# Kernel tuning notes

Measured on AMD Instinct MI355X. Metric: run time of the kernel, lower is better.

## Reference

```python
import jax, jax.numpy as jnp
import numpy as np

N_NODES = 100000
N_EDGES = 1600000
IN_CH = 128
NHIDDEN = 64
OUT_CH = 40
NLAYERS = 4
ALPHA = 0.1


def setup_inputs() -> dict:
    key = jax.random.key(0)
    ks = jax.random.split(key, 7)
    x = jax.random.normal(ks[0], (N_NODES, IN_CH), dtype=jnp.float32)
    edge_index = jax.random.randint(ks[1], (2, N_EDGES), 0, N_NODES, dtype=jnp.int64)
    batch_graph = jnp.zeros((N_NODES,), dtype=jnp.int64)
    fc1_w = jax.random.normal(ks[2], (NHIDDEN, IN_CH), dtype=jnp.float32) * (1.0 / np.sqrt(IN_CH))
    fc1_b = jax.random.normal(ks[3], (NHIDDEN,), dtype=jnp.float32) * 0.01
    conv_w = jax.random.normal(ks[4], (NLAYERS, NHIDDEN, NHIDDEN), dtype=jnp.float32) * (1.0 / np.sqrt(NHIDDEN))
    fc2_w = jax.random.normal(ks[5], (OUT_CH, NHIDDEN), dtype=jnp.float32) * (1.0 / np.sqrt(NHIDDEN))
    fc2_b = jax.random.normal(ks[6], (OUT_CH,), dtype=jnp.float32) * 0.01
    return {"x": x, "edge_index": edge_index, "batch_graph": batch_graph,
            "fc1_w": fc1_w, "fc1_b": fc1_b, "conv_w": conv_w,
            "fc2_w": fc2_w, "fc2_b": fc2_b}


def reference(x, edge_index, batch_graph, fc1_w, fc1_b, conv_w, fc2_w, fc2_b):
    # eval mode: dropout layers are identity
    n = x.shape[0]
    row, col = edge_index[0], edge_index[1]  # source, target

    # gcn_norm with add_self_loops=False: sym deg^-1/2 normalization
    deg = jax.ops.segment_sum(jnp.ones_like(row, dtype=x.dtype), col, num_segments=n)
    dinv = jnp.where(deg > 0, deg ** -0.5, 0.0)
    norm = (dinv[row] * dinv[col])[:, None]  # [E, 1]

    h = jax.nn.relu(x @ fc1_w.T + fc1_b)  # [N, nhidden]
    h0 = h
    nlayers = conv_w.shape[0]
    for i in range(nlayers):
        # GCN2Conv: aggregate, initial-residual mix, weight1 matmul (beta=1)
        agg = jax.ops.segment_sum(h[row] * norm, col, num_segments=n)
        mixed = (1.0 - ALPHA) * agg + ALPHA * h0
        h = jax.nn.relu(mixed @ conv_w[i])
    out = h @ fc2_w.T + fc2_b  # [N, out_channels]
    return out
```

## Files before the change

### kernel.cpp

```cpp
#include <hip/hip_runtime.h>
#include <hip/hip_fp16.h>

#define N_NODES 100000
#define N_EDGES 1600000
#define IN_CH   128
#define NHID    64
#define OUT_CH  40
#define NBLK    391
#define NBUCK   196
#define BCAP    8960


__global__ __launch_bounds__(256) void k_scan1(const int* __restrict__ cnt,
                                               int* __restrict__ rowptr,
                                               int* __restrict__ bsum) {
    __shared__ int s[256];
    int t = threadIdx.x;
    int n = blockIdx.x * 256 + t;
    int v = (n < N_NODES) ? cnt[n] : 0;
    s[t] = v;
    __syncthreads();
    for (int off = 1; off < 256; off <<= 1) {
        int add = (t >= off) ? s[t - off] : 0;
        __syncthreads();
        s[t] += add;
        __syncthreads();
    }
    int incl = s[t];
    if (n < N_NODES) rowptr[n] = incl - v;
    if (t == 255) bsum[blockIdx.x] = incl;
}

__global__ __launch_bounds__(512) void k_scan2(int* __restrict__ bsum) {
    __shared__ int s[512];
    int t = threadIdx.x;
    int v = (t < NBLK) ? bsum[t] : 0;
    s[t] = v;
    __syncthreads();
    for (int off = 1; off < 512; off <<= 1) {
        int add = (t >= off) ? s[t - off] : 0;
        __syncthreads();
        s[t] += add;
        __syncthreads();
    }
    if (t < NBLK) bsum[t] = s[t] - v;
}

__global__ __launch_bounds__(256) void k_scan3(const int* __restrict__ cnt,
                                               const int* __restrict__ bsum,
                                               int* __restrict__ rowptr,
                                               float* __restrict__ dinv) {
    int n = blockIdx.x * 256 + threadIdx.x;
    if (n < N_NODES) {
        int rp = rowptr[n] + bsum[n >> 8];
        rowptr[n] = rp;
        int c = cnt[n];
        dinv[n] = (c > 0) ? rsqrtf((float)c) : 0.0f;
    }
    if (blockIdx.x == 0 && threadIdx.x == 0) rowptr[N_NODES] = N_EDGES;
}


__global__ __launch_bounds__(256) void k_scatA(const int* __restrict__ ei,
                                               int* __restrict__ bucketCnt,
                                               int2* __restrict__ ebufA) {
    __shared__ int hist[NBUCK];
    __shared__ int base[NBUCK];
    int t = threadIdx.x;
    int chunk = blockIdx.x * 4096;
    for (int i = t; i < NBUCK; i += 256) hist[i] = 0;
    __syncthreads();
#pragma unroll 4
    for (int i = 0; i < 16; i++) {
        int e = chunk + i * 256 + t;
        if (e < N_EDGES) atomicAdd(&hist[ei[N_EDGES + e] >> 9], 1);
    }
    __syncthreads();
    for (int b = t; b < NBUCK; b += 256) {
        int h = hist[b];
        base[b] = h ? atomicAdd(&bucketCnt[b], h) : 0;
    }
    __syncthreads();
#pragma unroll 4
    for (int i = 0; i < 16; i++) {
        int e = chunk + i * 256 + t;
        if (e < N_EDGES) {
            int r = ei[e], c = ei[N_EDGES + e];
            int pos = atomicAdd(&base[c >> 9], 1);
            ebufA[(size_t)(c >> 9) * BCAP + pos] = make_int2(r, c);
        }
    }
}


__global__ __launch_bounds__(256) void k_deg(const int2* __restrict__ ebufA,
                                             const int* __restrict__ bucketCnt,
                                             int* __restrict__ cnt) {
    __shared__ int hist[512];
    int b = blockIdx.x;
    int nodeB = b * 512;
    int t = threadIdx.x;
    for (int i = t; i < 512; i += 256) hist[i] = 0;
    __syncthreads();
    int nE = bucketCnt[b];
    const int2* src = ebufA + (size_t)b * BCAP;
    for (int i = t; i < nE; i += 256) atomicAdd(&hist[src[i].y - nodeB], 1);
    __syncthreads();
    for (int i = t; i < 512; i += 256) {
        int node = nodeB + i;
        if (node < N_NODES) cnt[node] = hist[i];
    }
}


__global__ __launch_bounds__(256) void k_scatB(const int2* __restrict__ ebufA,
                                               const int* __restrict__ bucketCnt,
                                               const float* __restrict__ dinv,
                                               const int* __restrict__ rowptr,
                                               int2* __restrict__ e8) {
    __shared__ int lcur[512];
    int b = blockIdx.x;
    int nodeB = b * 512;
    int t = threadIdx.x;
    for (int i = t; i < 512; i += 256) {
        int node = nodeB + i;
        lcur[i] = (node < N_NODES) ? rowptr[node] : 0;
    }
    __syncthreads();
    int nE = bucketCnt[b];
    const int2* src = ebufA + (size_t)b * BCAP;
    for (int i = t; i < nE; i += 256) {
        int2 rc = src[i];
        float w = dinv[rc.x] * dinv[rc.y];
        int pos = atomicAdd(&lcur[rc.y - nodeB], 1);
        e8[pos] = make_int2(rc.x, __float_as_int(w));
    }
}

__device__ __forceinline__ void store_h4(__half* dst, float a, float b, float c, float d) {
    union { uint2 u; __half2 h[2]; } pk;
    pk.h[0] = __floats2half2_rn(a, b);
    pk.h[1] = __floats2half2_rn(c, d);
    *(uint2*)dst = pk.u;
}


__global__ __launch_bounds__(256, 4) void k_fc1(const float* __restrict__ x,
                                                const float* __restrict__ w,
                                                const float* __restrict__ b,
                                                float* __restrict__ h0,
                                                __half* __restrict__ h016) {
    __shared__ float xs[64 * 128];
    int t = threadIdx.x;
    int nodeBase = blockIdx.x * 64;

    {
        int nl = t >> 2, seg = t & 3;
        int n = nodeBase + nl;
        int swz = (nl >> 2) & 7;
        float4* dstrow = (float4*)(xs + nl * 128);
        if (n < N_NODES) {
            const float4* src = (const float4*)(x + (size_t)n * IN_CH + seg * 32);
#pragma unroll
            for (int q = 0; q < 8; q++) dstrow[(seg * 8 + q) ^ swz] = src[q];
        } else {
            float4 z = {0.f, 0.f, 0.f, 0.f};
#pragma unroll
            for (int q = 0; q < 8; q++) dstrow[(seg * 8 + q) ^ swz] = z;
        }
    }
    __syncthreads();

    int tx = t & 15, ty = t >> 4;
    int n0 = tx * 4, o0 = ty * 4;
    int swz = tx & 7;
    const float4* xrow0 = (const float4*)(xs + (n0 + 0) * 128);
    const float4* xrow1 = (const float4*)(xs + (n0 + 1) * 128);
    const float4* xrow2 = (const float4*)(xs + (n0 + 2) * 128);
    const float4* xrow3 = (const float4*)(xs + (n0 + 3) * 128);

    float c[4][4];
#pragma unroll
    for (int i = 0; i < 4; i++)
#pragma unroll
        for (int j = 0; j < 4; j++) c[i][j] = 0.f;

#pragma unroll 4
    for (int k = 0; k < IN_CH; k += 4) {
        int kg = (k >> 2) ^ swz;
        float4 b0 = *(const float4*)&w[(size_t)(o0 + 0) * IN_CH + k];
        float4 b1 = *(const float4*)&w[(size_t)(o0 + 1) * IN_CH + k];
        float4 b2 = *(const float4*)&w[(size_t)(o0 + 2) * IN_CH + k];
        float4 b3 = *(const float4*)&w[(size_t)(o0 + 3) * IN_CH + k];
        float4 a0 = xrow0[kg];
        float4 a1 = xrow1[kg];
        float4 a2 = xrow2[kg];
        float4 a3 = xrow3[kg];
#pragma unroll
        for (int i = 0; i < 4; i++) {
            float4 a = (i == 0) ? a0 : (i == 1) ? a1 : (i == 2) ? a2 : a3;
            c[i][0] = fmaf(a.x, b0.x, fmaf(a.y, b0.y, fmaf(a.z, b0.z, fmaf(a.w, b0.w, c[i][0]))));
            c[i][1] = fmaf(a.x, b1.x, fmaf(a.y, b1.y, fmaf(a.z, b1.z, fmaf(a.w, b1.w, c[i][1]))));
            c[i][2] = fmaf(a.x, b2.x, fmaf(a.y, b2.y, fmaf(a.z, b2.z, fmaf(a.w, b2.w, c[i][2]))));
            c[i][3] = fmaf(a.x, b3.x, fmaf(a.y, b3.y, fmaf(a.z, b3.z, fmaf(a.w, b3.w, c[i][3]))));
        }
    }

    float4 bias = *(const float4*)&b[o0];
#pragma unroll
    for (int i = 0; i < 4; i++) {
        int n = nodeBase + n0 + i;
        if (n < N_NODES) {
            float4 v;
            v.x = fmaxf(c[i][0] + bias.x, 0.f);
            v.y = fmaxf(c[i][1] + bias.y, 0.f);
            v.z = fmaxf(c[i][2] + bias.z, 0.f);
            v.w = fmaxf(c[i][3] + bias.w, 0.f);
            *(float4*)&h0[(size_t)n * NHID + o0] = v;
            store_h4(&h016[(size_t)n * NHID + o0], v.x, v.y, v.z, v.w);
        }
    }
}


__global__ __launch_bounds__(256, 4) void k_conv(const __half* __restrict__ hin,
                                                 const float* __restrict__ h0,
                                                 const int* __restrict__ rowptr,
                                                 const int2* __restrict__ e8,
                                                 const float* __restrict__ W,
                                                 __half* __restrict__ hout) {
    __shared__ float mix[32 * 68];
    int t = threadIdx.x;
    int nodeBase = blockIdx.x * 32;
    int grp = t >> 3;
    int cg = (t & 7) * 8;

    int n = nodeBase + grp;
    int s = rowptr[n], e = rowptr[n + 1];
    int d = e - s;
    int hi = (d > 0) ? (e - 1) : 0;

    float acc[8];
#pragma unroll
    for (int i = 0; i < 8; i++) acc[i] = 0.f;

    int2  pm[4];
    float4 pv[4];
    if (d > 0) {
#pragma unroll
        for (int u = 0; u < 4; u++) pm[u] = e8[min(s + u, hi)];
#pragma unroll
        for (int u = 0; u < 4; u++) pv[u] = *(const float4*)&hin[(size_t)pm[u].x * NHID + cg];
    }

    for (int j = s; j < e; j += 4) {
        int2  cm[4];
        float4 cv[4];
#pragma unroll
        for (int u = 0; u < 4; u++) { cm[u] = pm[u]; cv[u] = pv[u]; }
        int jn = j + 4;
        if (jn < e) {
#pragma unroll
            for (int u = 0; u < 4; u++) pm[u] = e8[min(jn + u, hi)];
#pragma unroll
            for (int u = 0; u < 4; u++) pv[u] = *(const float4*)&hin[(size_t)pm[u].x * NHID + cg];
        }
#pragma unroll
        for (int u = 0; u < 4; u++) {
            float wgt = (j + u < e) ? __int_as_float(cm[u].y) : 0.f;
            const __half2* hp = (const __half2*)&cv[u];
#pragma unroll
            for (int q = 0; q < 4; q++) {
                float2 f = __half22float2(hp[q]);
                acc[q * 2 + 0] = fmaf(wgt, f.x, acc[q * 2 + 0]);
                acc[q * 2 + 1] = fmaf(wgt, f.y, acc[q * 2 + 1]);
            }
        }
    }

    {
        float4 h0a = *(const float4*)&h0[(size_t)n * NHID + cg];
        float4 h0b = *(const float4*)&h0[(size_t)n * NHID + cg + 4];
        float4 m0, m1;
        m0.x = fmaf(0.9f, acc[0], 0.1f * h0a.x);
        m0.y = fmaf(0.9f, acc[1], 0.1f * h0a.y);
        m0.z = fmaf(0.9f, acc[2], 0.1f * h0a.z);
        m0.w = fmaf(0.9f, acc[3], 0.1f * h0a.w);
        m1.x = fmaf(0.9f, acc[4], 0.1f * h0b.x);
        m1.y = fmaf(0.9f, acc[5], 0.1f * h0b.y);
        m1.z = fmaf(0.9f, acc[6], 0.1f * h0b.z);
        m1.w = fmaf(0.9f, acc[7], 0.1f * h0b.w);
        *(float4*)&mix[grp * 68 + cg] = m0;
        *(float4*)&mix[grp * 68 + cg + 4] = m1;
    }
    __syncthreads();

    int tx = t & 15, ty = t >> 4;
    int o0 = tx * 4, r0 = ty * 2;
    float c[2][4];
#pragma unroll
    for (int i = 0; i < 2; i++)
#pragma unroll
        for (int j = 0; j < 4; j++) c[i][j] = 0.f;

#pragma unroll 4
    for (int k = 0; k < NHID; k += 4) {
        float4 b0 = *(const float4*)&W[(k + 0) * NHID + o0];
        float4 b1 = *(const float4*)&W[(k + 1) * NHID + o0];
        float4 b2 = *(const float4*)&W[(k + 2) * NHID + o0];
        float4 b3 = *(const float4*)&W[(k + 3) * NHID + o0];
#pragma unroll
        for (int i = 0; i < 2; i++) {
            float4 a = *(const float4*)&mix[(r0 + i) * 68 + k];
            c[i][0] = fmaf(a.x, b0.x, fmaf(a.y, b1.x, fmaf(a.z, b2.x, fmaf(a.w, b3.x, c[i][0]))));
            c[i][1] = fmaf(a.x, b0.y, fmaf(a.y, b1.y, fmaf(a.z, b2.y, fmaf(a.w, b3.y, c[i][1]))));
            c[i][2] = fmaf(a.x, b0.z, fmaf(a.y, b1.z, fmaf(a.z, b2.z, fmaf(a.w, b3.z, c[i][2]))));
            c[i][3] = fmaf(a.x, b0.w, fmaf(a.y, b1.w, fmaf(a.z, b2.w, fmaf(a.w, b3.w, c[i][3]))));
        }
    }
#pragma unroll
    for (int i = 0; i < 2; i++) {
        int n2 = nodeBase + r0 + i;
        store_h4(&hout[(size_t)n2 * NHID + o0],
                 fmaxf(c[i][0], 0.f), fmaxf(c[i][1], 0.f),
                 fmaxf(c[i][2], 0.f), fmaxf(c[i][3], 0.f));
    }
}


__global__ __launch_bounds__(256) void k_fc2(const __half* __restrict__ h,
                                             const float* __restrict__ w,
                                             const float* __restrict__ b,
                                             float* __restrict__ out) {
    __shared__ float wT[NHID * 44];
    __shared__ float hs[64 * 68];
    int t = threadIdx.x;
    int nodeBase = blockIdx.x * 64;

    for (int id = t; id < NHID * OUT_CH; id += 256) {
        int o = id >> 6, k = id & 63;
        wT[k * 44 + o] = w[id];
    }
    {
        int nl = t >> 2, seg = t & 3;
        int n = nodeBase + nl;
        float* dst = hs + nl * 68 + seg * 16;
        if (n < N_NODES) {
            float4 raw0 = *(const float4*)&h[(size_t)n * NHID + seg * 16];
            float4 raw1 = *(const float4*)&h[(size_t)n * NHID + seg * 16 + 8];
            const __half2* hp0 = (const __half2*)&raw0;
            const __half2* hp1 = (const __half2*)&raw1;
#pragma unroll
            for (int q = 0; q < 4; q++) {
                float2 f = __half22float2(hp0[q]);
                dst[q * 2 + 0] = f.x;
                dst[q * 2 + 1] = f.y;
            }
#pragma unroll
            for (int q = 0; q < 4; q++) {
                float2 f = __half22float2(hp1[q]);
                dst[8 + q * 2 + 0] = f.x;
                dst[8 + q * 2 + 1] = f.y;
            }
        } else {
#pragma unroll
            for (int q = 0; q < 16; q++) dst[q] = 0.f;
        }
    }
    __syncthreads();

    if (t < 160) {
        int tx = t % 10, ty = t / 10;
        int o0 = tx * 4, n0 = ty * 4;
        float c[4][4];
#pragma unroll
        for (int i = 0; i < 4; i++)
#pragma unroll
            for (int j = 0; j < 4; j++) c[i][j] = 0.f;

#pragma unroll 4
        for (int k = 0; k < NHID; k += 4) {
            float4 b0 = *(const float4*)&wT[(k + 0) * 44 + o0];
            float4 b1 = *(const float4*)&wT[(k + 1) * 44 + o0];
            float4 b2 = *(const float4*)&wT[(k + 2) * 44 + o0];
            float4 b3 = *(const float4*)&wT[(k + 3) * 44 + o0];
#pragma unroll
            for (int i = 0; i < 4; i++) {
                float4 a = *(const float4*)&hs[(n0 + i) * 68 + k];
                c[i][0] = fmaf(a.x, b0.x, fmaf(a.y, b1.x, fmaf(a.z, b2.x, fmaf(a.w, b3.x, c[i][0]))));
                c[i][1] = fmaf(a.x, b0.y, fmaf(a.y, b1.y, fmaf(a.z, b2.y, fmaf(a.w, b3.y, c[i][1]))));
                c[i][2] = fmaf(a.x, b0.z, fmaf(a.y, b1.z, fmaf(a.z, b2.z, fmaf(a.w, b3.z, c[i][2]))));
                c[i][3] = fmaf(a.x, b0.w, fmaf(a.y, b1.w, fmaf(a.z, b2.w, fmaf(a.w, b3.w, c[i][3]))));
            }
        }
        float4 bias = *(const float4*)&b[o0];
#pragma unroll
        for (int i = 0; i < 4; i++) {
            int n = nodeBase + n0 + i;
            if (n < N_NODES) {
                float4 v;
                v.x = c[i][0] + bias.x;
                v.y = c[i][1] + bias.y;
                v.z = c[i][2] + bias.z;
                v.w = c[i][3] + bias.w;
                *(float4*)&out[(size_t)n * OUT_CH + o0] = v;
            }
        }
    }
}


extern "C" void kernel_launch(void* const* d_in, const int* in_sizes, int n_in,
                              void* d_out, int out_size, void* d_ws, size_t ws_size,
                              hipStream_t stream) {
    const float* x    = (const float*)d_in[0];
    const int*   ei   = (const int*)d_in[1];
    const float* fc1w = (const float*)d_in[3];
    const float* fc1b = (const float*)d_in[4];
    const float* cw   = (const float*)d_in[5];
    const float* fc2w = (const float*)d_in[6];
    const float* fc2b = (const float*)d_in[7];
    float* out = (float*)d_out;

    char* p = (char*)d_ws;
    auto alloc = [&](size_t bytes) { char* r = p; p += (bytes + 255) & ~(size_t)255; return r; };
    float*  h0     = (float*) alloc((size_t)N_NODES * NHID * 4);
    __half* h016   = (__half*)alloc((size_t)N_NODES * NHID * 2);
    __half* ha16   = (__half*)alloc((size_t)N_NODES * NHID * 2);
    __half* hb16   = (__half*)alloc((size_t)N_NODES * NHID * 2);
    int2*   e8     = (int2*)  alloc(((size_t)N_EDGES + 8) * 8);
    int2*   ebufA  = (int2*)  alloc((size_t)NBUCK * BCAP * 8);
    int*    cnt    = (int*)   alloc((size_t)N_NODES * 4);
    int*    rowptr = (int*)   alloc((size_t)(N_NODES + 1) * 4);
    int*    bCnt   = (int*)   alloc((size_t)NBUCK * 4);
    float*  dinv   = (float*) alloc((size_t)N_NODES * 4);
    int*    bsum   = (int*)   alloc(512 * 4);

    hipMemsetAsync(bCnt, 0, (size_t)NBUCK * 4, stream);
    k_scatA<<<(N_EDGES + 4095) / 4096, 256, 0, stream>>>(ei, bCnt, ebufA);
    k_deg  <<<NBUCK, 256, 0, stream>>>(ebufA, bCnt, cnt);
    k_scan1<<<NBLK, 256, 0, stream>>>(cnt, rowptr, bsum);
    k_scan2<<<1, 512, 0, stream>>>(bsum);
    k_scan3<<<NBLK, 256, 0, stream>>>(cnt, bsum, rowptr, dinv);
    k_scatB<<<NBUCK, 256, 0, stream>>>(ebufA, bCnt, dinv, rowptr, e8);

    int gb64 = (N_NODES + 63) / 64;
    int gb32 = N_NODES / 32;
    k_fc1 <<<gb64, 256, 0, stream>>>(x, fc1w, fc1b, h0, h016);
    k_conv<<<gb32, 256, 0, stream>>>(h016, h0, rowptr, e8, cw + 0 * NHID * NHID, ha16);
    k_conv<<<gb32, 256, 0, stream>>>(ha16, h0, rowptr, e8, cw + 1 * NHID * NHID, hb16);
    k_conv<<<gb32, 256, 0, stream>>>(hb16, h0, rowptr, e8, cw + 2 * NHID * NHID, ha16);
    k_conv<<<gb32, 256, 0, stream>>>(ha16, h0, rowptr, e8, cw + 3 * NHID * NHID, hb16);
    k_fc2 <<<gb64, 256, 0, stream>>>(hb16, fc2w, fc2b, out);
}
```

Before: 440.2 us.

## Stage block edges in LDS, double-buffer gathers, fix fc1 LDS swizzle

```diff
diff --git a/kernel.cpp b/kernel.cpp
--- a/kernel.cpp
+++ b/kernel.cpp
@@ -9,6 +9,7 @@
 #define NBLK    391
 #define NBUCK   196
 #define BCAP    8960
+#define ECAP    1024
 
 
 __global__ __launch_bounds__(256) void k_scan1(const int* __restrict__ cnt,
@@ -157,7 +158,7 @@
     {
         int nl = t >> 2, seg = t & 3;
         int n = nodeBase + nl;
-        int swz = (nl >> 2) & 7;
+        int swz = (nl ^ (nl >> 3)) & 7;
         float4* dstrow = (float4*)(xs + nl * 128);
         if (n < N_NODES) {
             const float4* src = (const float4*)(x + (size_t)n * IN_CH + seg * 32);
@@ -173,7 +174,10 @@
 
     int tx = t & 15, ty = t >> 4;
     int n0 = tx * 4, o0 = ty * 4;
-    int swz = tx & 7;
+    int swz0 = ((n0 + 0) ^ ((n0 + 0) >> 3)) & 7;
+    int swz1 = ((n0 + 1) ^ ((n0 + 1) >> 3)) & 7;
+    int swz2 = ((n0 + 2) ^ ((n0 + 2) >> 3)) & 7;
+    int swz3 = ((n0 + 3) ^ ((n0 + 3) >> 3)) & 7;
     const float4* xrow0 = (const float4*)(xs + (n0 + 0) * 128);
     const float4* xrow1 = (const float4*)(xs + (n0 + 1) * 128);
     const float4* xrow2 = (const float4*)(xs + (n0 + 2) * 128);
@@ -187,15 +191,15 @@
 
 #pragma unroll 4
     for (int k = 0; k < IN_CH; k += 4) {
-        int kg = (k >> 2) ^ swz;
+        int kk = k >> 2;
         float4 b0 = *(const float4*)&w[(size_t)(o0 + 0) * IN_CH + k];
         float4 b1 = *(const float4*)&w[(size_t)(o0 + 1) * IN_CH + k];
         float4 b2 = *(const float4*)&w[(size_t)(o0 + 2) * IN_CH + k];
         float4 b3 = *(const float4*)&w[(size_t)(o0 + 3) * IN_CH + k];
-        float4 a0 = xrow0[kg];
-        float4 a1 = xrow1[kg];
-        float4 a2 = xrow2[kg];
-        float4 a3 = xrow3[kg];
+        float4 a0 = xrow0[kk ^ swz0];
+        float4 a1 = xrow1[kk ^ swz1];
+        float4 a2 = xrow2[kk ^ swz2];
+        float4 a3 = xrow3[kk ^ swz3];
 #pragma unroll
         for (int i = 0; i < 4; i++) {
             float4 a = (i == 0) ? a0 : (i == 1) ? a1 : (i == 2) ? a2 : a3;
@@ -229,54 +233,87 @@
                                                  const int2* __restrict__ e8,
                                                  const float* __restrict__ W,
                                                  __half* __restrict__ hout) {
+    __shared__ int2  eS[ECAP];
     __shared__ float mix[32 * 68];
     int t = threadIdx.x;
     int nodeBase = blockIdx.x * 32;
     int grp = t >> 3;
     int cg = (t & 7) * 8;
+
+    int base0 = rowptr[nodeBase];
+    int nE = rowptr[nodeBase + 32] - base0;
+    int nStage = (nE < ECAP) ? nE : ECAP;
+    for (int i = t; i < nStage; i += 256) eS[i] = e8[base0 + i];
 
     int n = nodeBase + grp;
     int s = rowptr[n], e = rowptr[n + 1];
     int d = e - s;
     int hi = (d > 0) ? (e - 1) : 0;
+    __syncthreads();
 
     float acc[8];
 #pragma unroll
     for (int i = 0; i < 8; i++) acc[i] = 0.f;
 
-    int2  pm[4];
-    float4 pv[4];
+#define LOADM(pm, jb)                                                    \
+    {                                                                    \
+        _Pragma("unroll")                                                \
+        for (int u = 0; u < 4; u++) {                                    \
+            int idx = min((jb) + u, hi);                                 \
+            int li = idx - base0;                                        \
+            if (li < ECAP) pm[u] = eS[li];                               \
+            else           pm[u] = e8[idx];                              \
+        }                                                                \
+    }
+#define ISSUE(pv, pm)                                                    \
+    {                                                                    \
+        _Pragma("unroll")                                                \
+        for (int u = 0; u < 4; u++)                                      \
+            pv[u] = *(const float4*)&hin[(size_t)pm[u].x * NHID + cg];   \
+    }
+#define FMA4(cm, cv, jb)                                                 \
+    {                                                                    \
+        _Pragma("unroll")                                                \
+        for (int u = 0; u < 4; u++) {                                    \
+            float wgt = ((jb) + u < e) ? __int_as_float(cm[u].y) : 0.f;  \
+            const __half2* hp = (const __half2*)&cv[u];                  \
+            _Pragma("unroll")                                            \
+            for (int q = 0; q < 4; q++) {                                \
+                float2 f = __half22float2(hp[q]);                        \
+                acc[q * 2 + 0] = fmaf(wgt, f.x, acc[q * 2 + 0]);         \
+                acc[q * 2 + 1] = fmaf(wgt, f.y, acc[q * 2 + 1]);         \
+            }                                                            \
+        }                                                                \
+    }
+
+    int2  pmA[4], pmB[4];
+    float4 pvA[4], pvB[4];
     if (d > 0) {
-#pragma unroll
-        for (int u = 0; u < 4; u++) pm[u] = e8[min(s + u, hi)];
-#pragma unroll
-        for (int u = 0; u < 4; u++) pv[u] = *(const float4*)&hin[(size_t)pm[u].x * NHID + cg];
-    }
-
-    for (int j = s; j < e; j += 4) {
-        int2  cm[4];
-        float4 cv[4];
-#pragma unroll
-        for (int u = 0; u < 4; u++) { cm[u] = pm[u]; cv[u] = pv[u]; }
-        int jn = j + 4;
-        if (jn < e) {
-#pragma unroll
-            for (int u = 0; u < 4; u++) pm[u] = e8[min(jn + u, hi)];
-#pragma unroll
-            for (int u = 0; u < 4; u++) pv[u] = *(const float4*)&hin[(size_t)pm[u].x * NHID + cg];
-        }
-#pragma unroll
-        for (int u = 0; u < 4; u++) {
-            float wgt = (j + u < e) ? __int_as_float(cm[u].y) : 0.f;
-            const __half2* hp = (const __half2*)&cv[u];
-#pragma unroll
-            for (int q = 0; q < 4; q++) {
-                float2 f = __half22float2(hp[q]);
-                acc[q * 2 + 0] = fmaf(wgt, f.x, acc[q * 2 + 0]);
-                acc[q * 2 + 1] = fmaf(wgt, f.y, acc[q * 2 + 1]);
-            }
-        }
-    }
+        LOADM(pmA, s);     ISSUE(pvA, pmA);
+        LOADM(pmB, s + 4); ISSUE(pvB, pmB);
+    }
+
+    for (int j = s; j < e; j += 8) {
+        {
+            int2 cm[4]; float4 cv[4];
+#pragma unroll
+            for (int u = 0; u < 4; u++) { cm[u] = pmA[u]; cv[u] = pvA[u]; }
+            int jn = j + 8;
+            if (jn < e) { LOADM(pmA, jn); ISSUE(pvA, pmA); }
+            FMA4(cm, cv, j);
+        }
+        if (j + 4 < e) {
+            int2 cm[4]; float4 cv[4];
+#pragma unroll
+            for (int u = 0; u < 4; u++) { cm[u] = pmB[u]; cv[u] = pvB[u]; }
+            int jn = j + 12;
+            if (jn < e) { LOADM(pmB, jn); ISSUE(pvB, pmB); }
+            FMA4(cm, cv, j + 4);
+        }
+    }
+#undef LOADM
+#undef ISSUE
+#undef FMA4
 
     {
         float4 h0a = *(const float4*)&h0[(size_t)n * NHID + cg];
```

Result: faster. 425.8 us (-3.3%).
